# Kernel tuning notes

Measured on AMD Instinct MI355X. Metric: run time of the kernel, lower is better.

## Reference

```python
import jax, jax.numpy as jnp
import numpy as np

CTX_WIN = 5
PAD = (CTX_WIN - 1) // 2


def setup_inputs() -> dict:
    key = jax.random.key(0)
    k1, k2, k3 = jax.random.split(key, 3)
    B, S, H, A = 64, 1024, 128, 8
    return {
        "batch_docIn": jax.random.normal(k1, (B, S, H), dtype=jnp.float32),
        "aspEmbed_weight": jax.random.uniform(k2, (A, CTX_WIN * H), dtype=jnp.float32, minval=-0.01, maxval=0.01),
        "aspProj": jax.random.uniform(k3, (A, H, H), dtype=jnp.float32, minval=-0.01, maxval=0.01),
    }


def reference(batch_docIn, aspEmbed_weight, aspProj):
    B, S, H = batch_docIn.shape
    A = aspProj.shape[0]
    # Per-aspect projection: (A, B, S, H)
    proj = jnp.einsum('bsh,ahf->absf', batch_docIn, aspProj)
    E = aspEmbed_weight.reshape(A, H, CTX_WIN)
    # Zero-pad along seq, then accumulate windowed scores without materializing
    padded = jnp.pad(proj, ((0, 0), (0, 0), (PAD, PAD), (0, 0)))
    attn = sum(
        jnp.einsum('absh,ah->abs',
                   jax.lax.dynamic_slice_in_dim(padded, w, S, axis=2),
                   E[:, :, w])
        for w in range(CTX_WIN)
    )  # (A, B, S)
    attn = jax.nn.softmax(attn, axis=2)  # softmax over seq (torch dim=1)
    rep = jnp.einsum('absh,abs->abh', proj, attn)  # (A, B, H)
    # outputs: attn (B, A, S), rep (B, A, H)
    return attn.transpose(1, 0, 2), rep.transpose(1, 0, 2)
```

## Files before the change

### kernel.cpp

```cpp
#include <hip/hip_runtime.h>
#include <hip/hip_bf16.h>

#define S_DIM 1024
#define H_DIM 128
#define A_DIM 8
#define W_WIN 5

typedef unsigned int uint;
typedef unsigned short ushort;
typedef __attribute__((ext_vector_type(8))) short short8;
typedef __attribute__((ext_vector_type(4))) float f32x4;

union U128 { uint4 u; short8 s; };

__device__ __forceinline__ ushort f2bf(float f) {
    uint u = __float_as_uint(f);
    uint r = (u + 0x7fffu + ((u >> 16) & 1u)) >> 16;
    return (ushort)r;
}

__global__ __launch_bounds__(128) void k_g(const float* __restrict__ P,
                                           const float* __restrict__ We,
                                           ushort* __restrict__ Gt) {
    const int a = blockIdx.x;
    const int h = threadIdx.x;
    if (a >= A_DIM) {
        for (int i = h; i < W_WIN * H_DIM; i += 128) Gt[a * (W_WIN * H_DIM) + i] = 0;
        return;
    }
    __shared__ float Es[H_DIM * W_WIN];
    for (int i = h; i < H_DIM * W_WIN; i += 128) Es[i] = We[a * (H_DIM * W_WIN) + i];
    __syncthreads();

    const float* Pr = P + ((size_t)a * H_DIM + h) * H_DIM;
    float acc[W_WIN] = {0.f, 0.f, 0.f, 0.f, 0.f};
#pragma unroll 8
    for (int f = 0; f < H_DIM; f += 4) {
        float4 pv = *(const float4*)(Pr + f);
        float pj[4] = {pv.x, pv.y, pv.z, pv.w};
#pragma unroll
        for (int j = 0; j < 4; ++j) {
            const float p = pj[j];
            const float* e = &Es[(f + j) * W_WIN];
#pragma unroll
            for (int w = 0; w < W_WIN; ++w) acc[w] += p * e[w];
        }
    }
#pragma unroll
    for (int w = 0; w < W_WIN; ++w)
        Gt[a * (W_WIN * H_DIM) + w * H_DIM + h] = f2bf(acc[w]);
}

#define CS 64
#define RROWS (CS + 4)
#define EPITCH 88
__global__ __launch_bounds__(256) void k_scores(const float* __restrict__ Din,
                                                const ushort* __restrict__ Gt,
                                                ushort* __restrict__ escore,
                                                float* __restrict__ numPart,
                                                float* __restrict__ Zpart) {
    __shared__ uint4 Dl[RROWS * 16];
    __shared__ uint4 Gl[9 * 80];
    __shared__ ushort el[16 * EPITCH];
    __shared__ float Zw[32];
    const int b   = blockIdx.y;
    const int slc = blockIdx.x;
    const int s0  = slc * CS;
    const int t   = threadIdx.x;
    const float* Db = Din + (size_t)b * S_DIM * H_DIM;

    for (int i = t; i < RROWS * 16; i += 256) {
        const int r = i >> 4, c = i & 15;
        const int gs = s0 - 2 + r;
        float4 va = make_float4(0.f, 0.f, 0.f, 0.f), vb = va;
        if (gs >= 0 && gs < S_DIM) {
            const float* p = Db + (size_t)gs * H_DIM + c * 8;
            va = ((const float4*)p)[0];
            vb = ((const float4*)p)[1];
        }
        uint4 q;
        q.x = (uint)f2bf(va.x) | ((uint)f2bf(va.y) << 16);
        q.y = (uint)f2bf(va.z) | ((uint)f2bf(va.w) << 16);
        q.z = (uint)f2bf(vb.x) | ((uint)f2bf(vb.y) << 16);
        q.w = (uint)f2bf(vb.z) | ((uint)f2bf(vb.w) << 16);
        Dl[r * 16 + (c ^ (r & 15))] = q;
    }
    {
        const uint4* Gg = (const uint4*)Gt;
        for (int i = t; i < 9 * 80; i += 256) {
            const int n = i / 80, c = i - n * 80;
            uint4 v = make_uint4(0u, 0u, 0u, 0u);
            if (n < 8) v = Gg[n * 80 + c];
            Gl[n * 80 + ((c & ~15) | ((c & 15) ^ n))] = v;
        }
    }
    __syncthreads();

    const int lane = t & 63;
    const int wv   = t >> 6;
    const int lm   = lane & 15;
    const int lq   = lane >> 4;
    const int gr   = (lm < 8) ? lm : 8;

    f32x4 acc0 = {0.f, 0.f, 0.f, 0.f};
#pragma unroll
    for (int kk = 0; kk < 20; ++kk) {
        const int w = kk >> 2;
        const int r0 = wv * 16 + lm + w;
        const int cidx = (kk & 3) * 4 + lq;
        const int gc = kk * 4 + lq;
        U128 av, bv;
        bv.u = Gl[gr * 80 + ((gc & ~15) | ((gc & 15) ^ gr))];
        av.u = Dl[r0 * 16 + (cidx ^ (r0 & 15))];
        acc0 = __builtin_amdgcn_mfma_f32_16x16x32_bf16(av.s, bv.s, acc0, 0, 0, 0);
    }

    float4 e0;
    e0.x = __expf(acc0.x); e0.y = __expf(acc0.y); e0.z = __expf(acc0.z); e0.w = __expf(acc0.w);
    uint2 d0;
    d0.x = (uint)f2bf(e0.x) | ((uint)f2bf(e0.y) << 16);
    d0.y = (uint)f2bf(e0.z) | ((uint)f2bf(e0.w) << 16);
    const int sb = wv * 16 + lq * 4;
    if (lm < A_DIM)
        *(uint2*)(escore + (((size_t)b * A_DIM + lm) << 10) + s0 + sb) = d0;
    *(uint2*)(&el[lm * EPITCH + sb]) = d0;

    float es = e0.x + e0.y + e0.z + e0.w;
    es += __shfl_xor(es, 16);
    es += __shfl_xor(es, 32);
    if (lq == 0 && lm < A_DIM) Zw[wv * 8 + lm] = es;
    __syncthreads();

    const ushort* Dls = (const ushort*)Dl;
    U128 afr[2];
#pragma unroll
    for (int kk = 0; kk < 2; ++kk)
        afr[kk].u = *(const uint4*)(&el[lm * EPITCH + kk * 32 + lq * 8]);

    f32x4 accN[2] = {{0.f,0.f,0.f,0.f},{0.f,0.f,0.f,0.f}};
#pragma unroll
    for (int nt = 0; nt < 2; ++nt) {
        const int h  = wv * 32 + nt * 16 + lm;
        const int ch = h >> 3, hw = h & 7;
#pragma unroll
        for (int kk = 0; kk < 2; ++kk) {
            uint p[4];
#pragma unroll
            for (int jj = 0; jj < 4; ++jj) {
                const int sj = kk * 32 + lq * 8 + jj * 2;
                const int ra = sj + 2, rb = sj + 3;
                const uint lo = Dls[(ra * 16 + (ch ^ (ra & 15))) * 8 + hw];
                const uint hi = Dls[(rb * 16 + (ch ^ (rb & 15))) * 8 + hw];
                p[jj] = lo | (hi << 16);
            }
            U128 bfr; bfr.u = make_uint4(p[0], p[1], p[2], p[3]);
            accN[nt] = __builtin_amdgcn_mfma_f32_16x16x32_bf16(afr[kk].s, bfr.s, accN[nt], 0, 0, 0);
        }
    }

    if (lq < 2) {
#pragma unroll
        for (int nt = 0; nt < 2; ++nt) {
            const int h = wv * 32 + nt * 16 + lm;
#pragma unroll
            for (int r = 0; r < 4; ++r)
                numPart[(((size_t)(b * 16 + slc) * 8) + lq * 4 + r) * H_DIM + h] = accN[nt][r];
        }
    }
    if (t < A_DIM)
        Zpart[(b * 16 + slc) * 8 + t] = Zw[t] + Zw[8 + t] + Zw[16 + t] + Zw[24 + t];
}

__global__ __launch_bounds__(128) void k_final(const ushort* __restrict__ escore,
                                               const float* __restrict__ numPart,
                                               const float* __restrict__ Zpart,
                                               const float* __restrict__ P,
                                               float* __restrict__ attn,
                                               float* __restrict__ rep) {
    __shared__ float ws[H_DIM];
    const int ba = blockIdx.x;
    const int b = ba >> 3, a = ba & 7;
    const int t = threadIdx.x;

    float Zs = 0.f;
#pragma unroll
    for (int k = 0; k < 16; ++k) Zs += Zpart[(b * 16 + k) * 8 + a];
    const float rz = 1.0f / Zs;

    float s = 0.f;
#pragma unroll
    for (int k = 0; k < 16; ++k)
        s += numPart[(((size_t)(b * 16 + k) * 8) + a) * H_DIM + t];
    ws[t] = s * rz;

    const ushort* ep = escore + (size_t)ba * S_DIM;
    float* ap = attn + (size_t)ba * S_DIM;
#pragma unroll
    for (int i = 0; i < 2; ++i) {
        uint2 q = *(const uint2*)(ep + i * 512 + t * 4);
        float4 v;
        v.x = __uint_as_float(q.x << 16) * rz;
        v.y = __uint_as_float(q.x & 0xffff0000u) * rz;
        v.z = __uint_as_float(q.y << 16) * rz;
        v.w = __uint_as_float(q.y & 0xffff0000u) * rz;
        *(float4*)(ap + i * 512 + t * 4) = v;
    }
    __syncthreads();

    const float* Pa = P + (size_t)a * H_DIM * H_DIM + t;
    float acc = 0.f;
#pragma unroll 32
    for (int hh = 0; hh < H_DIM; ++hh)
        acc += ws[hh] * Pa[(size_t)hh * H_DIM];
    rep[(size_t)ba * H_DIM + t] = acc;
}

extern "C" void kernel_launch(void* const* d_in, const int* in_sizes, int n_in,
                              void* d_out, int out_size, void* d_ws, size_t ws_size,
                              hipStream_t stream) {
    const float* docIn = (const float*)d_in[0];
    const float* We    = (const float*)d_in[1];
    const float* P     = (const float*)d_in[2];
    float* out = (float*)d_out;

    const int B = in_sizes[0] / (S_DIM * H_DIM);

    ushort* Gt     = (ushort*)d_ws;
    ushort* escore = (ushort*)((char*)d_ws + 32768);
    float* numPart = (float*)((char*)d_ws + 32768 +
                              (size_t)B * A_DIM * S_DIM * 2);
    float* Zpart   = numPart + (size_t)B * 16 * 8 * H_DIM;

    k_g<<<16, 128, 0, stream>>>(P, We, Gt);
    k_scores<<<dim3(S_DIM / CS, B), 256, 0, stream>>>(docIn, Gt, escore, numPart, Zpart);
    k_final<<<B * A_DIM, 128, 0, stream>>>(escore, numPart, Zpart, P, out,
                                           out + (size_t)B * A_DIM * S_DIM);
}
```

Before: 91.43 us.

## Fuse final normalization into scores kernel via last-block counter; split k_g

Removes the separate k_final launch. The last k_scores block to finish for each batch, detected with an atomic counter and threadfence, now reduces Z and the numerator partials, writes the normalized attn and computes rep. It also spreads the G-precompute across 64 blocks with a shared-memory reduction, which shortens its serial loop. The trade-off is that the finalization tail now runs on only 64 blocks, each doing eight times the work of an old k_final block, and adds an atomic plus fences.

```diff
diff --git a/kernel.cpp b/kernel.cpp
--- a/kernel.cpp
+++ b/kernel.cpp
@@ -21,34 +21,44 @@
 
 __global__ __launch_bounds__(128) void k_g(const float* __restrict__ P,
                                            const float* __restrict__ We,
-                                           ushort* __restrict__ Gt) {
-    const int a = blockIdx.x;
-    const int h = threadIdx.x;
-    if (a >= A_DIM) {
-        for (int i = h; i < W_WIN * H_DIM; i += 128) Gt[a * (W_WIN * H_DIM) + i] = 0;
-        return;
-    }
+                                           ushort* __restrict__ Gt,
+                                           int* __restrict__ done) {
+    const int a  = blockIdx.y;
+    const int hc = blockIdx.x;
+    const int t  = threadIdx.x;
+
+    if (a == 0 && hc == 0 && t < 64) done[t] = 0;
+
     __shared__ float Es[H_DIM * W_WIN];
-    for (int i = h; i < H_DIM * W_WIN; i += 128) Es[i] = We[a * (H_DIM * W_WIN) + i];
-    __syncthreads();
-
-    const float* Pr = P + ((size_t)a * H_DIM + h) * H_DIM;
+    __shared__ float red[16 * 8 * W_WIN];
+    for (int i = t; i < H_DIM * W_WIN; i += 128) Es[i] = We[a * (H_DIM * W_WIN) + i];
+    __syncthreads();
+
+    const int hl = t >> 3, fo = t & 7;
+    const float* Pr = P + ((size_t)(a * H_DIM + hc * 16 + hl)) * H_DIM + fo * 16;
     float acc[W_WIN] = {0.f, 0.f, 0.f, 0.f, 0.f};
-#pragma unroll 8
-    for (int f = 0; f < H_DIM; f += 4) {
-        float4 pv = *(const float4*)(Pr + f);
+#pragma unroll
+    for (int j4 = 0; j4 < 4; ++j4) {
+        float4 pv = ((const float4*)Pr)[j4];
         float pj[4] = {pv.x, pv.y, pv.z, pv.w};
 #pragma unroll
         for (int j = 0; j < 4; ++j) {
-            const float p = pj[j];
-            const float* e = &Es[(f + j) * W_WIN];
-#pragma unroll
-            for (int w = 0; w < W_WIN; ++w) acc[w] += p * e[w];
-        }
-    }
-#pragma unroll
-    for (int w = 0; w < W_WIN; ++w)
-        Gt[a * (W_WIN * H_DIM) + w * H_DIM + h] = f2bf(acc[w]);
+            const float* e = &Es[(fo * 16 + j4 * 4 + j) * W_WIN];
+#pragma unroll
+            for (int w = 0; w < W_WIN; ++w) acc[w] += pj[j] * e[w];
+        }
+    }
+#pragma unroll
+    for (int w = 0; w < W_WIN; ++w) red[(hl * 8 + fo) * W_WIN + w] = acc[w];
+    __syncthreads();
+
+    if (t < 80) {
+        const int w = t >> 4, h2 = t & 15;
+        float s = 0.f;
+#pragma unroll
+        for (int f8 = 0; f8 < 8; ++f8) s += red[(h2 * 8 + f8) * W_WIN + w];
+        Gt[a * (W_WIN * H_DIM) + w * H_DIM + hc * 16 + h2] = f2bf(s);
+    }
 }
 
 #define CS 64
@@ -58,11 +68,16 @@
                                                 const ushort* __restrict__ Gt,
                                                 ushort* __restrict__ escore,
                                                 float* __restrict__ numPart,
-                                                float* __restrict__ Zpart) {
+                                                float* __restrict__ Zpart,
+                                                const float* __restrict__ P,
+                                                float* __restrict__ attn,
+                                                float* __restrict__ rep,
+                                                int* __restrict__ done) {
     __shared__ uint4 Dl[RROWS * 16];
     __shared__ uint4 Gl[9 * 80];
     __shared__ ushort el[16 * EPITCH];
     __shared__ float Zw[32];
+    __shared__ int lastFlag;
     const int b   = blockIdx.y;
     const int slc = blockIdx.x;
     const int s0  = slc * CS;
@@ -169,50 +184,55 @@
     }
     if (t < A_DIM)
         Zpart[(b * 16 + slc) * 8 + t] = Zw[t] + Zw[8 + t] + Zw[16 + t] + Zw[24 + t];
-}
-
-__global__ __launch_bounds__(128) void k_final(const ushort* __restrict__ escore,
-                                               const float* __restrict__ numPart,
-                                               const float* __restrict__ Zpart,
-                                               const float* __restrict__ P,
-                                               float* __restrict__ attn,
-                                               float* __restrict__ rep) {
-    __shared__ float ws[H_DIM];
-    const int ba = blockIdx.x;
-    const int b = ba >> 3, a = ba & 7;
-    const int t = threadIdx.x;
-
-    float Zs = 0.f;
-#pragma unroll
-    for (int k = 0; k < 16; ++k) Zs += Zpart[(b * 16 + k) * 8 + a];
-    const float rz = 1.0f / Zs;
-
-    float s = 0.f;
-#pragma unroll
-    for (int k = 0; k < 16; ++k)
-        s += numPart[(((size_t)(b * 16 + k) * 8) + a) * H_DIM + t];
-    ws[t] = s * rz;
-
-    const ushort* ep = escore + (size_t)ba * S_DIM;
-    float* ap = attn + (size_t)ba * S_DIM;
-#pragma unroll
-    for (int i = 0; i < 2; ++i) {
-        uint2 q = *(const uint2*)(ep + i * 512 + t * 4);
+
+    __syncthreads();
+    if (t == 0) {
+        __threadfence();
+        lastFlag = (atomicAdd(&done[b], 1) == 15);
+    }
+    __syncthreads();
+    if (!lastFlag) return;
+    __threadfence();
+
+    float* fs = (float*)Dl;
+    float* Zf = (float*)Gl;
+    if (t < A_DIM) {
+        float z = 0.f;
+#pragma unroll
+        for (int k = 0; k < 16; ++k) z += Zpart[(b * 16 + k) * 8 + t];
+        Zf[t] = 1.0f / z;
+    }
+    for (int i = t; i < A_DIM * H_DIM; i += 256) {
+        float s = 0.f;
+#pragma unroll
+        for (int k = 0; k < 16; ++k)
+            s += numPart[(((size_t)(b * 16 + k) * 8) + (i >> 7)) * H_DIM + (i & 127)];
+        fs[i] = s;
+    }
+    __syncthreads();
+
+    for (int i = t; i < (A_DIM * S_DIM) / 4; i += 256) {
+        const int a2 = i >> 8;
+        const float rz = Zf[a2];
+        const size_t off = (((size_t)b * 8 + a2) << 10) + ((i & 255) << 2);
+        uint2 q = *(const uint2*)(escore + off);
         float4 v;
         v.x = __uint_as_float(q.x << 16) * rz;
         v.y = __uint_as_float(q.x & 0xffff0000u) * rz;
         v.z = __uint_as_float(q.y << 16) * rz;
         v.w = __uint_as_float(q.y & 0xffff0000u) * rz;
-        *(float4*)(ap + i * 512 + t * 4) = v;
-    }
-    __syncthreads();
-
-    const float* Pa = P + (size_t)a * H_DIM * H_DIM + t;
-    float acc = 0.f;
-#pragma unroll 32
-    for (int hh = 0; hh < H_DIM; ++hh)
-        acc += ws[hh] * Pa[(size_t)hh * H_DIM];
-    rep[(size_t)ba * H_DIM + t] = acc;
+        *(float4*)(attn + off) = v;
+    }
+
+    for (int i = t; i < A_DIM * H_DIM; i += 256) {
+        const int a2 = i >> 7, f = i & 127;
+        const float* Pa = P + (size_t)a2 * H_DIM * H_DIM + f;
+        float acc = 0.f;
+#pragma unroll 16
+        for (int hh = 0; hh < H_DIM; ++hh)
+            acc += fs[(a2 << 7) + hh] * Pa[(size_t)hh * H_DIM];
+        rep[(((size_t)b * 8 + a2)) * H_DIM + f] = acc * Zf[a2];
+    }
 }
 
 extern "C" void kernel_launch(void* const* d_in, const int* in_sizes, int n_in,
@@ -226,13 +246,15 @@
     const int B = in_sizes[0] / (S_DIM * H_DIM);
 
     ushort* Gt     = (ushort*)d_ws;
+    int*    done   = (int*)((char*)d_ws + 20480);
     ushort* escore = (ushort*)((char*)d_ws + 32768);
     float* numPart = (float*)((char*)d_ws + 32768 +
                               (size_t)B * A_DIM * S_DIM * 2);
     float* Zpart   = numPart + (size_t)B * 16 * 8 * H_DIM;
 
-    k_g<<<16, 128, 0, stream>>>(P, We, Gt);
-    k_scores<<<dim3(S_DIM / CS, B), 256, 0, stream>>>(docIn, Gt, escore, numPart, Zpart);
-    k_final<<<B * A_DIM, 128, 0, stream>>>(escore, numPart, Zpart, P, out,
-                                           out + (size_t)B * A_DIM * S_DIM);
-}
+    k_g<<<dim3(8, 8), 128, 0, stream>>>(P, We, Gt, done);
+    k_scores<<<dim3(S_DIM / CS, B), 256, 0, stream>>>(docIn, Gt, escore, numPart, Zpart,
+                                                      P, out,
+                                                      out + (size_t)B * A_DIM * S_DIM,
+                                                      done);
+}
```

New measurement: 150.4 us. 64.5% more time.

## Parallelize k_g and k_final across more blocks and batch k_scores input loads

Applied to the files above, without the earlier changes.

k_g is split into an 8x8 grid: each block handles 16 output rows, and the reduction over f is shared across 8 threads with a final shared-memory sum. This shortens a long serial loop that ran on only a few blocks. k_final now runs two blocks per (b,a) pair, each covering half of rep's output columns, with the h reduction split across two thread halves. k_scores issues all its global loads up front using clamped addresses, which gives more memory-level parallelism before the bf16 conversion. The costs are redundant Z and ws computation in k_final and a few extra reduction syncs.

```diff
diff --git a/kernel.cpp b/kernel.cpp
--- a/kernel.cpp
+++ b/kernel.cpp
@@ -22,33 +22,40 @@
 __global__ __launch_bounds__(128) void k_g(const float* __restrict__ P,
                                            const float* __restrict__ We,
                                            ushort* __restrict__ Gt) {
-    const int a = blockIdx.x;
-    const int h = threadIdx.x;
-    if (a >= A_DIM) {
-        for (int i = h; i < W_WIN * H_DIM; i += 128) Gt[a * (W_WIN * H_DIM) + i] = 0;
-        return;
-    }
+    const int a  = blockIdx.y;
+    const int hc = blockIdx.x;
+    const int t  = threadIdx.x;
+
     __shared__ float Es[H_DIM * W_WIN];
-    for (int i = h; i < H_DIM * W_WIN; i += 128) Es[i] = We[a * (H_DIM * W_WIN) + i];
-    __syncthreads();
-
-    const float* Pr = P + ((size_t)a * H_DIM + h) * H_DIM;
+    __shared__ float red[16 * 8 * W_WIN];
+    for (int i = t; i < H_DIM * W_WIN; i += 128) Es[i] = We[a * (H_DIM * W_WIN) + i];
+    __syncthreads();
+
+    const int hl = t >> 3, fo = t & 7;
+    const float* Pr = P + ((size_t)(a * H_DIM + hc * 16 + hl)) * H_DIM + fo * 16;
     float acc[W_WIN] = {0.f, 0.f, 0.f, 0.f, 0.f};
-#pragma unroll 8
-    for (int f = 0; f < H_DIM; f += 4) {
-        float4 pv = *(const float4*)(Pr + f);
+#pragma unroll
+    for (int j4 = 0; j4 < 4; ++j4) {
+        float4 pv = ((const float4*)Pr)[j4];
         float pj[4] = {pv.x, pv.y, pv.z, pv.w};
 #pragma unroll
         for (int j = 0; j < 4; ++j) {
-            const float p = pj[j];
-            const float* e = &Es[(f + j) * W_WIN];
-#pragma unroll
-            for (int w = 0; w < W_WIN; ++w) acc[w] += p * e[w];
-        }
-    }
-#pragma unroll
-    for (int w = 0; w < W_WIN; ++w)
-        Gt[a * (W_WIN * H_DIM) + w * H_DIM + h] = f2bf(acc[w]);
+            const float* e = &Es[(fo * 16 + j4 * 4 + j) * W_WIN];
+#pragma unroll
+            for (int w = 0; w < W_WIN; ++w) acc[w] += pj[j] * e[w];
+        }
+    }
+#pragma unroll
+    for (int w = 0; w < W_WIN; ++w) red[(hl * 8 + fo) * W_WIN + w] = acc[w];
+    __syncthreads();
+
+    if (t < 80) {
+        const int w = t >> 4, h2 = t & 15;
+        float s = 0.f;
+#pragma unroll
+        for (int f8 = 0; f8 < 8; ++f8) s += red[(h2 * 8 + f8) * W_WIN + w];
+        Gt[a * (W_WIN * H_DIM) + w * H_DIM + hc * 16 + h2] = f2bf(s);
+    }
 }
 
 #define CS 64
@@ -69,21 +76,41 @@
     const int t   = threadIdx.x;
     const float* Db = Din + (size_t)b * S_DIM * H_DIM;
 
-    for (int i = t; i < RROWS * 16; i += 256) {
-        const int r = i >> 4, c = i & 15;
-        const int gs = s0 - 2 + r;
-        float4 va = make_float4(0.f, 0.f, 0.f, 0.f), vb = va;
-        if (gs >= 0 && gs < S_DIM) {
-            const float* p = Db + (size_t)gs * H_DIM + c * 8;
-            va = ((const float4*)p)[0];
-            vb = ((const float4*)p)[1];
-        }
-        uint4 q;
-        q.x = (uint)f2bf(va.x) | ((uint)f2bf(va.y) << 16);
-        q.y = (uint)f2bf(va.z) | ((uint)f2bf(va.w) << 16);
-        q.z = (uint)f2bf(vb.x) | ((uint)f2bf(vb.y) << 16);
-        q.w = (uint)f2bf(vb.z) | ((uint)f2bf(vb.w) << 16);
-        Dl[r * 16 + (c ^ (r & 15))] = q;
+    {
+        const int c  = t & 15;
+        const int r0 = t >> 4;
+        float4 va[5], vb[5];
+        bool ok[5];
+#pragma unroll
+        for (int k = 0; k < 4; ++k) {
+            const int gs = s0 - 2 + r0 + k * 16;
+            ok[k] = (gs >= 0) && (gs < S_DIM);
+            const int gc = min(max(gs, 0), S_DIM - 1);
+            const float4* p = (const float4*)(Db + (size_t)gc * H_DIM + c * 8);
+            va[k] = p[0];
+            vb[k] = p[1];
+        }
+        if (t < 64) {
+            const int gs = s0 - 2 + 64 + r0;
+            ok[4] = (gs >= 0) && (gs < S_DIM);
+            const int gc = min(max(gs, 0), S_DIM - 1);
+            const float4* p = (const float4*)(Db + (size_t)gc * H_DIM + c * 8);
+            va[4] = p[0];
+            vb[4] = p[1];
+        }
+#pragma unroll
+        for (int k = 0; k < 5; ++k) {
+            if (k == 4 && t >= 64) break;
+            const int r = (k == 4) ? (64 + r0) : (r0 + k * 16);
+            float4 A = va[k], Bv = vb[k];
+            if (!ok[k]) { A = make_float4(0.f,0.f,0.f,0.f); Bv = A; }
+            uint4 q;
+            q.x = (uint)f2bf(A.x)  | ((uint)f2bf(A.y)  << 16);
+            q.y = (uint)f2bf(A.z)  | ((uint)f2bf(A.w)  << 16);
+            q.z = (uint)f2bf(Bv.x) | ((uint)f2bf(Bv.y) << 16);
+            q.w = (uint)f2bf(Bv.z) | ((uint)f2bf(Bv.w) << 16);
+            Dl[r * 16 + (c ^ (r & 15))] = q;
+        }
     }
     {
         const uint4* Gg = (const uint4*)Gt;
@@ -178,7 +205,9 @@
                                                float* __restrict__ attn,
                                                float* __restrict__ rep) {
     __shared__ float ws[H_DIM];
-    const int ba = blockIdx.x;
+    __shared__ float par[128];
+    const int ba = blockIdx.y;
+    const int hf = blockIdx.x;
     const int b = ba >> 3, a = ba & 7;
     const int t = threadIdx.x;
 
@@ -195,24 +224,28 @@
 
     const ushort* ep = escore + (size_t)ba * S_DIM;
     float* ap = attn + (size_t)ba * S_DIM;
-#pragma unroll
-    for (int i = 0; i < 2; ++i) {
-        uint2 q = *(const uint2*)(ep + i * 512 + t * 4);
+    {
+        uint2 q = *(const uint2*)(ep + hf * 512 + t * 4);
         float4 v;
         v.x = __uint_as_float(q.x << 16) * rz;
         v.y = __uint_as_float(q.x & 0xffff0000u) * rz;
         v.z = __uint_as_float(q.y << 16) * rz;
         v.w = __uint_as_float(q.y & 0xffff0000u) * rz;
-        *(float4*)(ap + i * 512 + t * 4) = v;
-    }
-    __syncthreads();
-
-    const float* Pa = P + (size_t)a * H_DIM * H_DIM + t;
+        *(float4*)(ap + hf * 512 + t * 4) = v;
+    }
+    __syncthreads();
+
+    const int f  = hf * 64 + (t & 63);
+    const int h0 = (t >> 6) * 64;
+    const float* Pa = P + (size_t)a * H_DIM * H_DIM + f;
     float acc = 0.f;
-#pragma unroll 32
-    for (int hh = 0; hh < H_DIM; ++hh)
-        acc += ws[hh] * Pa[(size_t)hh * H_DIM];
-    rep[(size_t)ba * H_DIM + t] = acc;
+#pragma unroll 16
+    for (int hh = 0; hh < 64; ++hh)
+        acc += ws[h0 + hh] * Pa[(size_t)(h0 + hh) * H_DIM];
+    par[t] = acc;
+    __syncthreads();
+    if (t < 64)
+        rep[(size_t)ba * H_DIM + f] = par[t] + par[t + 64];
 }
 
 extern "C" void kernel_launch(void* const* d_in, const int* in_sizes, int n_in,
@@ -231,8 +264,8 @@
                               (size_t)B * A_DIM * S_DIM * 2);
     float* Zpart   = numPart + (size_t)B * 16 * 8 * H_DIM;
 
-    k_g<<<16, 128, 0, stream>>>(P, We, Gt);
+    k_g<<<dim3(8, 8), 128, 0, stream>>>(P, We, Gt);
     k_scores<<<dim3(S_DIM / CS, B), 256, 0, stream>>>(docIn, Gt, escore, numPart, Zpart);
-    k_final<<<B * A_DIM, 128, 0, stream>>>(escore, numPart, Zpart, P, out,
-                                           out + (size_t)B * A_DIM * S_DIM);
-}
+    k_final<<<dim3(2, B * A_DIM), 128, 0, stream>>>(escore, numPart, Zpart, P, out,
+                                                    out + (size_t)B * A_DIM * S_DIM);
+}
```

Measured after the change: 89.10 us. 1.03x faster.
